# Kernel optimization log

Hardware: AMD Instinct MI355X
Metric: run time of the kernel (lower is better)

Reference implementation:

```python
import jax, jax.numpy as jnp
import numpy as np

NODE_FEAT = 200  # F.interpolate size in run_all_node
TOPN = 2         # StitchModel.topn


def _node_feats(img, mask, flow, n_inst, max_pix):
    """Vectorized run_all_node: per-instance gather, linear interp to NODE_FEAT,
    3x3 sign histogram of flow[:2], mean of flow[2]. mask holds labels 1..n_inst;
    max_pix is a static upper bound on pixels per instance."""
    flat = mask.reshape(-1) - 1                       # labels 0..N-1
    order = jnp.argsort(flat)                         # stable sort by label
    counts = jax.ops.segment_sum(jnp.ones_like(flat), flat, num_segments=n_inst)
    starts = jnp.concatenate([jnp.zeros((1,), counts.dtype), jnp.cumsum(counts)[:-1]])
    j = jnp.arange(max_pix)
    pos = starts[:, None] + jnp.minimum(j[None, :], counts[:, None] - 1)
    idx = order[pos]                                  # [N, max_pix] padded pixel indices
    valid = j[None, :] < counts[:, None]              # [N, max_pix]
    iv = img.reshape(-1)[idx]                         # instance intensity profiles
    fx = flow[0].reshape(-1)[idx]
    fy = flow[1].reshape(-1)[idx]
    fz = flow[2].reshape(-1)[idx]
    cf = counts.astype(img.dtype)
    zflow = jnp.where(valid, fz, 0).sum(1) / cf       # flows[-1][m].mean()

    def interp(v, L):                                 # torch linear interp, align_corners=False
        Lf = L.astype(img.dtype)
        p = jnp.clip((jnp.arange(NODE_FEAT, dtype=img.dtype) + 0.5) * (Lf / NODE_FEAT) - 0.5,
                     0.0, Lf - 1.0)
        i0 = jnp.floor(p).astype(jnp.int32)
        i1 = jnp.minimum(i0 + 1, L - 1)
        w = p - i0.astype(img.dtype)
        return v[i0] * (1 - w) + v[i1] * w

    nodes = jax.vmap(interp)(iv, counts)              # [N, 200]
    # hist_flow_vector: bins ordered (x:<0,==0,>0) x (y:<0,==0,>0) -> 3*cx+cy
    cx = jnp.where(fx < 0, 0, jnp.where(fx == 0, 1, 2))
    cy = jnp.where(fy < 0, 0, jnp.where(fy == 0, 1, 2))
    bins = cx * 3 + cy
    oh = (bins[..., None] == jnp.arange(9)) & valid[..., None]
    hist = oh.sum(1).astype(img.dtype)                # [N, 9]
    return jnp.concatenate([nodes, hist], -1), zflow


def setup_inputs() -> dict:
    H = W = 2048
    N = 4096
    pix = (H * W) // N
    key = jax.random.key(0)
    ks = jax.random.split(key, 8)

    def make_mask(k):
        labels = (jnp.arange(H * W, dtype=jnp.int32) // pix) + 1   # labels 1..N
        perm = jax.random.permutation(k, H * W)
        return labels[perm].reshape(H, W)

    def make_bbox(k):
        u = jax.random.uniform(k, (N, 4), jnp.float32)
        centers = u[:, :2] * H
        sizes = u[:, 2:] * 49.0 + 1.0                               # nonzero w/h (asserted)
        return jnp.concatenate([centers, sizes], -1)

    return {
        "img1": jax.random.normal(ks[0], (H, W), jnp.float32),
        "img2": jax.random.normal(ks[1], (H, W), jnp.float32),
        "flow1": jax.random.normal(ks[2], (3, H, W), jnp.float32),
        "flow2": jax.random.normal(ks[3], (3, H, W), jnp.float32),
        "bbox1": make_bbox(ks[4]),
        "bbox2": make_bbox(ks[5]),
        "mask1": make_mask(ks[6]),
        "mask2": make_mask(ks[7]),
    }


def reference(img1, img2, flow1, flow2, bbox1, bbox2, mask1, mask2):
    N1, N2 = bbox1.shape[0], bbox2.shape[0]
    max1 = mask1.size // N1   # static bound on pixels/instance (equal-partition masks)
    max2 = mask2.size // N2
    node1, zf1 = _node_feats(img1, mask1, flow1, N1, max1)
    node2, zf2 = _node_feats(img2, mask2, flow2, N2, max2)
    x = jnp.concatenate([node1, node2], 0)            # [(N1+N2), 209]
    # build_one_graph_low_ram: per row, TOPN smallest center distances
    d = jnp.sqrt(((bbox1[:, None, :2] - bbox2[None, :, :2]) ** 2).sum(-1))  # [N1,N2]
    _, nbr = jax.lax.top_k(-d, TOPN)                  # smallest-first, like argsort[:topn]
    src = jnp.repeat(jnp.arange(N1), TOPN)            # [N1*TOPN]
    dst = nbr.reshape(-1)
    edge_index = jnp.stack([src, dst + N1])           # [2, N1*TOPN]
    edge_attr = jnp.stack([
        zf1[src], zf2[dst],
        bbox1[src, 0] - bbox2[dst, 0],
        bbox1[src, 1] - bbox2[dst, 1],
        bbox1[src, 2] / bbox2[dst, 2],
        bbox1[src, 3] / bbox2[dst, 3],
    ], -1)                                            # [N1*TOPN, 6]
    return x, edge_index, edge_attr
```

## Files before the change

### kernel.cpp

```cpp
#include <hip/hip_runtime.h>
#include <math.h>

#pragma clang fp contract(off)

#define HW      (2048*2048)
#define NI      4096
#define MAXPIX  1024
#define NF      200
#define FEAT    209
#define NE      (NI*2)
#define XSIZE   ((2*NI)*FEAT)
#define EIOFF   XSIZE
#define EAOFF   (EIOFF + 2*NE)

#define S       8192
#define CHK     (HW/S)
#define TOTCHK  (2*CHK)
#define NBPI    256
#define LPB     16
#define NBG     (2*NBPI)
#define REC     (2*HW)
#define BTOT    (LPB*MAXPIX)
#define NWS     16

template<int NB>
__device__ __forceinline__ unsigned long long match_bits(int v) {
    unsigned long long m = ~0ull;
    #pragma unroll
    for (int bit = 0; bit < NB; ++bit) {
        unsigned long long bb = __ballot((v >> bit) & 1);
        m &= ((v >> bit) & 1) ? bb : ~bb;
    }
    return m;
}

__global__ void __launch_bounds__(512) count_zf_kernel(const int* __restrict__ mask1,
        const int* __restrict__ mask2, const float* __restrict__ flow1,
        const float* __restrict__ flow2, unsigned* __restrict__ cntA,
        float* __restrict__ zfpart) {
    __shared__ unsigned cnt[8][NBPI];
    __shared__ float zfp[NI];
    int t = threadIdx.x, w = t >> 6, lane = t & 63;
    for (int j = t; j < 8*NBPI; j += 512) ((unsigned*)cnt)[j] = 0u;
    for (int j = t; j < NI; j += 512) zfp[j] = 0.f;
    __syncthreads();
    int c = blockIdx.x;
    int img = c / CHK;
    const int4*   mask  = (const int4*)(img ? mask2 : mask1);
    const float4* flowz = (const float4*)((img ? flow2 : flow1) + 2L*HW);
    long base4 = (long)(c - img*CHK) * (S/4) + (long)w * (S/32);
    #pragma unroll
    for (int it = 0; it < S/32; it += 64) {
        int4   l4 = mask[base4 + it + lane];
        float4 fz = flowz[base4 + it + lane];
        atomicAdd(&cnt[w][(l4.x-1) >> 4], 1u);
        atomicAdd(&cnt[w][(l4.y-1) >> 4], 1u);
        atomicAdd(&cnt[w][(l4.z-1) >> 4], 1u);
        atomicAdd(&cnt[w][(l4.w-1) >> 4], 1u);
        atomicAdd(&zfp[l4.x-1], fz.x);
        atomicAdd(&zfp[l4.y-1], fz.y);
        atomicAdd(&zfp[l4.z-1], fz.z);
        atomicAdd(&zfp[l4.w-1], fz.w);
    }
    __syncthreads();
    if (t < NBPI) {
        unsigned s = 0;
        #pragma unroll
        for (int q = 0; q < 8; ++q) s += cnt[q][t];
        cntA[(long)c * NBPI + t] = s;
    }
    float* zdst = zfpart + (long)c * NI;
    for (int j = t; j < NI; j += 512) zdst[j] = zfp[j];
}

__global__ void __launch_bounds__(256) scan1_zf_kernel(unsigned* __restrict__ cntA,
        const float* __restrict__ zfpart, float* __restrict__ zfm) {
    __shared__ int wsum[4];
    __shared__ float zpar[16][LPB];
    int gb = blockIdx.x;
    int img = gb >> 8, lb = gb & (NBPI - 1);
    int t = threadIdx.x, lane = t & 63, w = t >> 6;
    const int PER = CHK / 256;
    unsigned e[PER]; int s = 0;
    long base = ((long)img * CHK + (long)t * PER) * NBPI + lb;
    #pragma unroll
    for (int i = 0; i < PER; ++i) { e[i] = cntA[base + (long)i * NBPI]; s += (int)e[i]; }
    int incl = s;
    #pragma unroll
    for (int off = 1; off < 64; off <<= 1) {
        int o = __shfl_up(incl, off);
        if (lane >= off) incl += o;
    }
    if (lane == 63) wsum[w] = incl;
    __syncthreads();
    int add = 0;
    for (int q = 0; q < w; ++q) add += wsum[q];
    unsigned pre = (unsigned)(incl + add - s);
    #pragma unroll
    for (int i = 0; i < PER; ++i) { unsigned cv = e[i]; cntA[base + (long)i * NBPI] = pre; pre += cv; }
    {
        int l0 = (gb * LPB) & (NI-1);
        int lab = t & 15, rg = t >> 4;
        const float* zp = zfpart + ((long)img*CHK + rg*32)*NI + l0 + lab;
        float s32 = 0.f;
        #pragma unroll
        for (int k = 0; k < 32; ++k) s32 += zp[(long)k*NI];
        zpar[rg][lab] = s32;
    }
    __syncthreads();
    if (t < LPB) {
        float sum = 0.f;
        #pragma unroll
        for (int g = 0; g < 16; ++g) sum += zpar[g][t];
        zfm[gb*LPB + t] = sum * (1.0f/(float)MAXPIX);
    }
}

__global__ void __launch_bounds__(1024, 8) sort_kernel(
        const float* __restrict__ img1, const float* __restrict__ img2,
        const float* __restrict__ flow1, const float* __restrict__ flow2,
        const int* __restrict__ mask1, const int* __restrict__ mask2,
        const unsigned* __restrict__ cntA,
        float* __restrict__ riv, unsigned char* __restrict__ rmeta) {
    __shared__ float ivs[S];
    __shared__ unsigned short smeta[S];
    __shared__ unsigned short cw[NWS][NBPI];
    int* wsum  = (int*)smeta;
    int* gofsA = (int*)cw;
    int t = threadIdx.x, w = t >> 6, lane = t & 63;
    int c = blockIdx.x;
    int img = c / CHK;
    const int*   mask  = img ? mask2  : mask1;
    const float* image = img ? img2   : img1;
    const float* flow  = img ? flow2  : flow1;
    long base = (long)(c - img*CHK) * S;
    unsigned pre = 0;
    if (t < NBPI) pre = cntA[(long)c * NBPI + t];
    for (int j = t; j < NWS*NBPI; j += 1024) ((unsigned short*)cw)[j] = 0;
    __syncthreads();
    long qbase = base + (long)w * (S/NWS);
    int   pk[8];
    float piv[8];
    unsigned long long ltmask = (1ull << lane) - 1ull;
    #pragma unroll
    for (int it = 0; it < 8; ++it) {
        long p = qbase + it*64 + lane;
        int l = mask[p] - 1;
        piv[it] = image[p];
        float fx = flow[p], fy = flow[HW + p];
        int cx = fx < 0.f ? 0 : (fx == 0.f ? 1 : 2);
        int cy = fy < 0.f ? 0 : (fy == 0.f ? 1 : 2);
        int bkt = l >> 4;
        unsigned long long m = match_bits<8>(bkt);
        int cb = __popcll(m & ltmask);
        int ct = __popcll(m);
        pk[it] = l | ((cx*3 + cy) << 12) | (cb << 16) | (ct << 22);
        if (cb == 0) cw[w][bkt] += (unsigned short)ct;
    }
    __syncthreads();
    int tot = 0, incl = 0;
    if (t < NBPI) {
        #pragma unroll
        for (int q = 0; q < NWS; ++q) tot += cw[q][t];
        incl = tot;
        #pragma unroll
        for (int off = 1; off < 64; off <<= 1) {
            int o = __shfl_up(incl, off);
            if (lane >= off) incl += o;
        }
        if (lane == 63) wsum[w] = incl;
    }
    __syncthreads();
    int gof = 0;
    if (t < NBPI) {
        int add = 0;
        for (int q = 0; q < w; ++q) add += wsum[q];
        int excl = incl + add - tot;
        int run = excl;
        #pragma unroll
        for (int q = 0; q < NWS; ++q) {
            int cq = cw[q][t];
            cw[q][t] = (unsigned short)run;
            run += cq;
        }
        gof = (img*NBPI + t) * BTOT + (int)pre - excl;
    }
    __syncthreads();
    #pragma unroll
    for (int it = 0; it < 8; ++it) {
        int pkv = pk[it];
        int l = pkv & 4095, bin = (pkv >> 12) & 15;
        int cb = (pkv >> 16) & 63, ct = (pkv >> 22) & 127;
        int bkt = l >> 4;
        int r0 = (int)cw[w][bkt];
        int dst = r0 + cb;
        if (cb == ct - 1) cw[w][bkt] = (unsigned short)(r0 + ct);
        ivs[dst] = piv[it];
        smeta[dst] = (unsigned short)((bkt << 8) | (bin << 4) | (l & 15));
    }
    __syncthreads();
    if (t < NBPI) gofsA[t] = gof;
    __syncthreads();
    for (int j = t; j < S; j += 1024) {
        int ms = (int)smeta[j];
        int b = ms >> 8;
        int g = gofsA[b] + j;
        riv[g]   = ivs[j];
        rmeta[g] = (unsigned char)(ms & 0xFF);
    }
}

__global__ void __launch_bounds__(1024) stageB_kernel(
        const float* __restrict__ riv, const unsigned char* __restrict__ rmeta,
        float* __restrict__ out) {
    __shared__ float acc[LPB * NF];
    __shared__ float s_tw[MAXPIX];
    __shared__ int   s_tk[MAXPIX];
    __shared__ int   hist[LPB * 9];
    __shared__ int   qc[16][LPB];
    __shared__ int   cur[16][LPB];
    int t = threadIdx.x, w = t >> 6, lane = t & 63;
    int gb = blockIdx.x;
    for (int j = t; j < LPB*NF; j += 1024) acc[j] = 0.f;
    if (t < MAXPIX) s_tk[t] = -1;
    if (t < LPB*9) hist[t] = 0;
    for (int j = t; j < 16*LPB; j += 1024) ((int*)qc)[j] = 0;
    __syncthreads();
    if (t < NF) {
        const float Lf = (float)MAXPIX;
        float p = ((float)t + 0.5f) * (Lf / (float)NF) - 0.5f;
        p = fminf(fmaxf(p, 0.0f), Lf - 1.0f);
        int i0 = (int)floorf(p);
        int i1 = min(i0 + 1, MAXPIX - 1);
        float wg = p - (float)i0;
        s_tk[i0] = t; s_tw[i0] = 1.0f - wg;
        s_tk[i1] = t; s_tw[i1] = wg;
    }
    long base = (long)gb * BTOT;
    const int qsz = BTOT / 16;
    int qbeg = w * qsz;
    const int nit = qsz / 64;
    unsigned long long ltmask = (1ull << lane) - 1ull;
    {
        const uchar4* rm4 = (const uchar4*)(rmeta + base + qbeg);
        #pragma unroll
        for (int it = 0; it < nit/4; ++it) {
            uchar4 m = rm4[it*64 + lane];
            atomicAdd(&qc[w][m.x & 15], 1);
            atomicAdd(&qc[w][m.y & 15], 1);
            atomicAdd(&qc[w][m.z & 15], 1);
            atomicAdd(&qc[w][m.w & 15], 1);
        }
    }
    __syncthreads();
    if (t < LPB) {
        int s = 0;
        #pragma unroll
        for (int q = 0; q < 16; ++q) { cur[q][t] = s; s += qc[q][t]; }
    }
    __syncthreads();
    #pragma unroll 4
    for (int it = 0; it < nit; ++it) {
        int i = qbeg + it*64 + lane;
        int meta = (int)rmeta[base + i];
        float iv = riv[base + i];
        int ll = meta & 15;
        unsigned long long m = match_bits<4>(ll);
        int cb = __popcll(m & ltmask);
        int ct = __popcll(m);
        int r0 = cur[w][ll];
        int rank = r0 + cb;
        if (cb == ct - 1) cur[w][ll] = r0 + ct;
        atomicAdd(&hist[ll*9 + (meta >> 4)], 1);
        int k = s_tk[rank];
        if (k >= 0) atomicAdd(&acc[ll*NF + k], iv * s_tw[rank]);
    }
    __syncthreads();
    for (int j = t; j < LPB*FEAT; j += 1024) {
        int r = j / FEAT, k = j - r*FEAT;
        float v = (k < NF) ? acc[r*NF + k] : (float)hist[r*9 + (k - NF)];
        out[(long)gb * LPB * FEAT + j] = v;
    }
}

__device__ __forceinline__ bool better(float d, int j, float d2, int j2) {
    return d < d2 || (d == d2 && j < j2);
}

__global__ void __launch_bounds__(256) edge_kernel(const float* __restrict__ bbox1,
                                                   const float* __restrict__ bbox2,
                                                   const float* __restrict__ zfm,
                                                   float* __restrict__ out) {
    __shared__ float sbx[NI], sby[NI];
    int wave = threadIdx.x >> 6, lane = threadIdx.x & 63;
    for (int r = threadIdx.x; r < NI; r += 256) {
        float4 b = ((const float4*)bbox2)[r];
        sbx[r] = b.x; sby[r] = b.y;
    }
    __syncthreads();
    int i = blockIdx.x * 4 + wave;
    float c1x = bbox1[i*4 + 0], c1y = bbox1[i*4 + 1];
    float d0 = INFINITY; int j0 = 0x7fffffff;
    float d1 = INFINITY; int j1 = 0x7fffffff;
    for (int t = 0; t < NI; t += 64) {
        int j = t + lane;
        float dx = c1x - sbx[j];
        float dy = c1y - sby[j];
        float dsq = dx*dx + dy*dy;
        float d = (float)sqrt((double)dsq);
        if (better(d, j, d0, j0)) { d1 = d0; j1 = j0; d0 = d; j0 = j; }
        else if (better(d, j, d1, j1)) { d1 = d; j1 = j; }
    }
    for (int off = 32; off; off >>= 1) {
        float od0 = __shfl_down(d0, off); int oj0 = __shfl_down(j0, off);
        float od1 = __shfl_down(d1, off); int oj1 = __shfl_down(j1, off);
        if (better(od0, oj0, d0, j0)) {
            if (better(d0, j0, od1, oj1)) { d1 = d0; j1 = j0; }
            else                          { d1 = od1; j1 = oj1; }
            d0 = od0; j0 = oj0;
        } else if (better(od0, oj0, d1, j1)) { d1 = od0; j1 = oj0; }
    }
    if (lane == 0) {
        float z1 = zfm[i];
        int js[2] = { j0, j1 };
        for (int t = 0; t < 2; ++t) {
            int e = i*2 + t, j = js[t];
            out[EIOFF + e]      = (float)i;
            out[EIOFF + NE + e] = (float)(j + NI);
            float* ea = out + EAOFF + (long)e * 6;
            ea[0] = z1;
            ea[1] = zfm[NI + j];
            ea[2] = c1x - bbox2[j*4 + 0];
            ea[3] = c1y - bbox2[j*4 + 1];
            ea[4] = bbox1[i*4 + 2] / bbox2[j*4 + 2];
            ea[5] = bbox1[i*4 + 3] / bbox2[j*4 + 3];
        }
    }
}

extern "C" void kernel_launch(void* const* d_in, const int* in_sizes, int n_in,
                              void* d_out, int out_size, void* d_ws, size_t ws_size,
                              hipStream_t stream) {
    const float* img1  = (const float*)d_in[0];
    const float* img2  = (const float*)d_in[1];
    const float* flow1 = (const float*)d_in[2];
    const float* flow2 = (const float*)d_in[3];
    const float* bbox1 = (const float*)d_in[4];
    const float* bbox2 = (const float*)d_in[5];
    const int*   mask1 = (const int*)d_in[6];
    const int*   mask2 = (const int*)d_in[7];
    float* out = (float*)d_out;

    char* ws = (char*)d_ws;
    size_t off = 0;
    unsigned* cntA   = (unsigned*)(ws + off); off += (size_t)TOTCHK * NBPI * 4;
    float*    riv    = (float*)(ws + off);    off += (size_t)REC * 4;
    float*    zfpart = (float*)(ws + off);    off += (size_t)TOTCHK * NI * 4;
    float*    zfm    = (float*)(ws + off);    off += 2 * NI * 4;
    unsigned char* rmeta = (unsigned char*)(ws + off); off += (size_t)REC;

    hipLaunchKernelGGL(count_zf_kernel, dim3(TOTCHK), dim3(512), 0, stream,
                       mask1, mask2, flow1, flow2, cntA, zfpart);
    hipLaunchKernelGGL(scan1_zf_kernel, dim3(NBG), dim3(256), 0, stream,
                       cntA, zfpart, zfm);
    hipLaunchKernelGGL(sort_kernel, dim3(TOTCHK), dim3(1024), 0, stream,
                       img1, img2, flow1, flow2, mask1, mask2, cntA, riv, rmeta);
    hipLaunchKernelGGL(stageB_kernel, dim3(NBG), dim3(1024), 0, stream,
                       riv, rmeta, out);
    hipLaunchKernelGGL(edge_kernel, dim3(NI/4), dim3(256), 0, stream,
                       bbox1, bbox2, zfm, out);
}
```

Measured before the change: 301.5 us.

## Split zflow reduction into separate kernel and swizzle sort blocks across XCDs

Moves the per-label zflow partial-sum reduction out of the scan kernel into its own kernel. The new kernel uses 1024-thread blocks whose lanes read contiguous 64-label rows, so the 16 MB of partials is read with coalesced accesses instead of 16-wide strided reads. The sort kernel also remaps block IDs so that consecutive chunks land on the same XCD, which is meant to improve L2 locality for the cntA and mask reads. The cost is one extra kernel launch, and the chunk remap changes the order in which blocks are scheduled.

```diff
diff --git a/kernel.cpp b/kernel.cpp
--- a/kernel.cpp
+++ b/kernel.cpp
@@ -22,6 +22,7 @@
 #define REC     (2*HW)
 #define BTOT    (LPB*MAXPIX)
 #define NWS     16
+#define NXCD    8
 
 template<int NB>
 __device__ __forceinline__ unsigned long long match_bits(int v) {
@@ -73,10 +74,8 @@
     for (int j = t; j < NI; j += 512) zdst[j] = zfp[j];
 }
 
-__global__ void __launch_bounds__(256) scan1_zf_kernel(unsigned* __restrict__ cntA,
-        const float* __restrict__ zfpart, float* __restrict__ zfm) {
+__global__ void __launch_bounds__(256) scan1_kernel(unsigned* __restrict__ cntA) {
     __shared__ int wsum[4];
-    __shared__ float zpar[16][LPB];
     int gb = blockIdx.x;
     int img = gb >> 8, lb = gb & (NBPI - 1);
     int t = threadIdx.x, lane = t & 63, w = t >> 6;
@@ -98,21 +97,26 @@
     unsigned pre = (unsigned)(incl + add - s);
     #pragma unroll
     for (int i = 0; i < PER; ++i) { unsigned cv = e[i]; cntA[base + (long)i * NBPI] = pre; pre += cv; }
-    {
-        int l0 = (gb * LPB) & (NI-1);
-        int lab = t & 15, rg = t >> 4;
-        const float* zp = zfpart + ((long)img*CHK + rg*32)*NI + l0 + lab;
-        float s32 = 0.f;
-        #pragma unroll
-        for (int k = 0; k < 32; ++k) s32 += zp[(long)k*NI];
-        zpar[rg][lab] = s32;
-    }
-    __syncthreads();
-    if (t < LPB) {
+}
+
+__global__ void __launch_bounds__(1024) zfred_kernel(const float* __restrict__ zfpart,
+        float* __restrict__ zfm) {
+    __shared__ float red[16][64];
+    int t = threadIdx.x, b = blockIdx.x;
+    int img = b >> 6;
+    int l0  = (b & 63) * 64;
+    int rg = t >> 6, lane = t & 63;
+    const float* p = zfpart + ((long)img*CHK + rg)*NI + l0 + lane;
+    float s = 0.f;
+    #pragma unroll 8
+    for (int r = 0; r < CHK; r += 16) s += p[(long)r*NI];
+    red[rg][lane] = s;
+    __syncthreads();
+    if (t < 64) {
         float sum = 0.f;
         #pragma unroll
-        for (int g = 0; g < 16; ++g) sum += zpar[g][t];
-        zfm[gb*LPB + t] = sum * (1.0f/(float)MAXPIX);
+        for (int g = 0; g < 16; ++g) sum += red[g][t];
+        zfm[img*NI + l0 + t] = sum * (1.0f/(float)MAXPIX);
     }
 }
 
@@ -128,7 +132,8 @@
     int* wsum  = (int*)smeta;
     int* gofsA = (int*)cw;
     int t = threadIdx.x, w = t >> 6, lane = t & 63;
-    int c = blockIdx.x;
+    int bid = blockIdx.x;
+    int c = (bid & (NXCD-1)) * (TOTCHK/NXCD) + (bid >> 3);
     int img = c / CHK;
     const int*   mask  = img ? mask2  : mask1;
     const float* image = img ? img2   : img1;
@@ -361,8 +366,8 @@
 
     hipLaunchKernelGGL(count_zf_kernel, dim3(TOTCHK), dim3(512), 0, stream,
                        mask1, mask2, flow1, flow2, cntA, zfpart);
-    hipLaunchKernelGGL(scan1_zf_kernel, dim3(NBG), dim3(256), 0, stream,
-                       cntA, zfpart, zfm);
+    hipLaunchKernelGGL(scan1_kernel, dim3(NBG), dim3(256), 0, stream, cntA);
+    hipLaunchKernelGGL(zfred_kernel, dim3(128), dim3(1024), 0, stream, zfpart, zfm);
     hipLaunchKernelGGL(sort_kernel, dim3(TOTCHK), dim3(1024), 0, stream,
                        img1, img2, flow1, flow2, mask1, mask2, cntA, riv, rmeta);
     hipLaunchKernelGGL(stageB_kernel, dim3(NBG), dim3(1024), 0, stream,
```

Result: no change. 302.3 us (+0.3%).
